# Kernel tuning notes

Hardware: AMD Instinct MI355X
Metric: run time of the kernel (lower is better)

The kernel has to match this reference:

```python
import jax, jax.numpy as jnp
import numpy as np

N = 16384
D = 512
NNZ = 163840
NUM_ITERS = 10


def setup_inputs() -> dict:
    key = jax.random.key(0)
    k1, k2, k3, k4 = jax.random.split(key, 4)
    x = jax.random.normal(k1, (N, D), dtype=jnp.float32)
    edge_val = jax.random.uniform(k2, (NNZ,), dtype=jnp.float32)
    edge_row = jnp.sort(jax.random.randint(k3, (NNZ,), 0, N, dtype=jnp.int32))
    edge_col = jax.random.randint(k4, (NNZ,), 0, N, dtype=jnp.int32)
    alpha = jnp.zeros((1,), dtype=jnp.float32)
    beta = jnp.zeros((1,), dtype=jnp.float32)
    sigma = jnp.ones((1,), dtype=jnp.float32)
    return {"x": x, "alpha": alpha, "beta": beta, "sigma": sigma,
            "edge_val": edge_val, "edge_row": edge_row, "edge_col": edge_col,
            "num_iters": NUM_ITERS}


def reference(x, alpha, beta, sigma, edge_val, edge_row, edge_col, num_iters):
    n = x.shape[0]
    # tf.nn.l2_normalize(x, axis=1)
    xn = x * jax.lax.rsqrt(jnp.maximum(jnp.sum(x * x, axis=1, keepdims=True), 1e-12))
    # cosine similarity only at sparse support positions; diagonal zeroed
    sim_e = jnp.sum(xn[edge_row] * xn[edge_col], axis=-1)          # [nnz]
    sim_e = jnp.where(edge_row == edge_col, 0.0, sim_e)
    s = jnp.exp(sigma[0])
    sigma_sq = 2.0 * s * s
    sim_e = jnp.exp(sim_e / (2.0 * sigma_sq))
    # support = sparse support elementwise * similarity
    sup = edge_val * sim_e                                          # [nnz]
    # row-sum of sparse support
    normalize = jax.ops.segment_sum(sup, edge_row, num_segments=n)  # [N]
    a = jnp.exp(alpha[0])
    b = jnp.exp(beta[0])
    denom = b + normalize[:, None] * a + a                          # [N,1] -> broadcast over D

    def step(out, _):
        # sparse matmul: (support @ out)
        Ax = jax.ops.segment_sum(sup[:, None] * out[edge_col], edge_row, num_segments=n)
        out = (x * b + (Ax + out) * a) / denom
        return out, None

    out, _ = jax.lax.scan(step, x, None, length=num_iters)
    return out
```

## Files before the change

kernel.cpp:

```cpp
#include <hip/hip_runtime.h>
#include <hip/hip_fp16.h>

#define DIM 512
#define N_ITERS 10

typedef float floatx2 __attribute__((ext_vector_type(2)));
typedef float fx4 __attribute__((ext_vector_type(4)));
typedef unsigned int ux4 __attribute__((ext_vector_type(4)));

__device__ __forceinline__ unsigned int pack2h(float lo, float hi) {
    __half2 h = __float22half2_rn(make_float2(lo, hi));
    return *reinterpret_cast<unsigned int*>(&h);
}
__device__ __forceinline__ float2 unpack2h(unsigned int u) {
    return __half22float2(*reinterpret_cast<__half2*>(&u));
}
__device__ __forceinline__ unsigned int pack4f8(float f0, float f1, float f2, float f3) {
    int v = 0;
    v = __builtin_amdgcn_cvt_pk_fp8_f32(f0, f1, v, false);
    v = __builtin_amdgcn_cvt_pk_fp8_f32(f2, f3, v, true);
    return (unsigned int)v;
}

__global__ void __launch_bounds__(256)
prep_kernel(const float* __restrict__ x,
            const float* __restrict__ alpha,
            const float* __restrict__ beta,
            const float* __restrict__ sigma,
            const int* __restrict__ erow, int nnz,
            float* __restrict__ consts,
            int* __restrict__ rstart,
            unsigned int* __restrict__ xc8,
            unsigned short* __restrict__ xbh, int n) {
    int tid = blockIdx.x * blockDim.x + threadIdx.x;
    float b = expf(beta[0]);
    if (tid == 0) {
        float a = expf(alpha[0]);
        float s = expf(sigma[0]);
        consts[0] = a;
        consts[1] = b;
        consts[2] = 1.0f / (4.0f * s * s);
    }
    if (tid <= n) {
        int lo = 0, hi = nnz;
        while (lo < hi) {
            int mid = (lo + hi) >> 1;
            if (erow[mid] < tid) lo = mid + 1; else hi = mid;
        }
        rstart[tid] = lo;
    }
    int wid = tid >> 6;
    int lane = tid & 63;
    if (wid >= n) return;
    const size_t base = (size_t)wid * DIM + lane * 8;
    const fx4* p = (const fx4*)(x + base);
    fx4 u = p[0];
    fx4 v = p[1];
    float s = u.x*u.x + u.y*u.y + u.z*u.z + u.w*u.w
            + v.x*v.x + v.y*v.y + v.z*v.z + v.w*v.w;
    ux4 hb;
    hb.x = pack2h(u.x * b, u.y * b); hb.y = pack2h(u.z * b, u.w * b);
    hb.z = pack2h(v.x * b, v.y * b); hb.w = pack2h(v.z * b, v.w * b);
    *(ux4*)(xbh + base) = hb;
    #pragma unroll
    for (int m = 32; m >= 1; m >>= 1) s += __shfl_xor(s, m, 64);
    float inr = rsqrtf(fmaxf(s, 1e-12f));
    ux4 q;
    q.x = pack4f8(u.x * inr, u.y * inr, u.z * inr, u.w * inr);
    q.y = pack4f8(v.x * inr, v.y * inr, v.z * inr, v.w * inr);
    q.z = pack4f8(u.x, u.y, u.z, u.w);
    q.w = pack4f8(v.x, v.y, v.z, v.w);
    *(ux4*)(xc8 + ((size_t)wid * 256 + lane * 4)) = q;
}

__device__ __forceinline__ float dot8f8(const float* A, unsigned int lo, unsigned int hi) {
    floatx2 p0 = __builtin_amdgcn_cvt_pk_f32_fp8((int)lo, false);
    floatx2 p1 = __builtin_amdgcn_cvt_pk_f32_fp8((int)lo, true);
    floatx2 p2 = __builtin_amdgcn_cvt_pk_f32_fp8((int)hi, false);
    floatx2 p3 = __builtin_amdgcn_cvt_pk_f32_fp8((int)hi, true);
    return A[0]*p0.x + A[1]*p0.y + A[2]*p1.x + A[3]*p1.y
         + A[4]*p2.x + A[5]*p2.y + A[6]*p3.x + A[7]*p3.y;
}

#define ACCP(lo, hi, w2)                                                          \
    do {                                                                          \
        acc0 += (w2) * __builtin_amdgcn_cvt_pk_f32_fp8((int)(lo), false);         \
        acc1 += (w2) * __builtin_amdgcn_cvt_pk_f32_fp8((int)(lo), true);          \
        acc2 += (w2) * __builtin_amdgcn_cvt_pk_f32_fp8((int)(hi), false);         \
        acc3 += (w2) * __builtin_amdgcn_cvt_pk_f32_fp8((int)(hi), true);          \
    } while (0)

__global__ void __launch_bounds__(256)
fused1_kernel(const unsigned int* __restrict__ xc8,
              const float* __restrict__ x,
              const float* __restrict__ eval_,
              const int* __restrict__ ecol,
              const int* __restrict__ rstart,
              const float* __restrict__ consts,
              float* __restrict__ sup, float* __restrict__ inv_denom,
              unsigned short* __restrict__ next16,
              unsigned int* __restrict__ next8, int n) {
    int row = (blockIdx.x * blockDim.x + threadIdx.x) >> 6;
    int lane = threadIdx.x & 63;
    if (row >= n) return;
    const size_t base = (size_t)row * DIM + lane * 8;
    ux4 hr = *(const ux4*)(xc8 + (size_t)row * 256 + lane * 4);
    const fx4* px = (const fx4*)(x + base);
    fx4 u = px[0];
    fx4 v = px[1];
    float A[8];
    {
        floatx2 p0 = __builtin_amdgcn_cvt_pk_f32_fp8((int)hr.x, false);
        floatx2 p1 = __builtin_amdgcn_cvt_pk_f32_fp8((int)hr.x, true);
        floatx2 p2 = __builtin_amdgcn_cvt_pk_f32_fp8((int)hr.y, false);
        floatx2 p3 = __builtin_amdgcn_cvt_pk_f32_fp8((int)hr.y, true);
        A[0]=p0.x; A[1]=p0.y; A[2]=p1.x; A[3]=p1.y;
        A[4]=p2.x; A[5]=p2.y; A[6]=p3.x; A[7]=p3.y;
    }
    float a = consts[0], b = consts[1], c2 = consts[2];
    int rs = rstart[row], re = rstart[row + 1];
    float norm_acc = 0.0f;
    floatx2 acc0 = {0.f, 0.f}, acc1 = {0.f, 0.f}, acc2 = {0.f, 0.f}, acc3 = {0.f, 0.f};
    int e = rs;
    for (; e + 3 < re; e += 4) {
        int c[4]; float ev[4]; ux4 h[4]; float s[4];
        #pragma unroll
        for (int j = 0; j < 4; ++j) { c[j] = ecol[e + j]; ev[j] = eval_[e + j]; }
        #pragma unroll
        for (int j = 0; j < 4; ++j)
            h[j] = *(const ux4*)(xc8 + (size_t)c[j] * 256 + lane * 4);
        #pragma unroll
        for (int j = 0; j < 4; ++j) s[j] = dot8f8(A, h[j].x, h[j].y);
        #pragma unroll
        for (int m = 32; m >= 1; m >>= 1) {
            #pragma unroll
            for (int j = 0; j < 4; ++j) s[j] += __shfl_xor(s[j], m, 64);
        }
        #pragma unroll
        for (int j = 0; j < 4; ++j) {
            float sim = (row == c[j]) ? 0.0f : s[j];
            float sp = ev[j] * expf(sim * c2);
            norm_acc += sp;
            if (lane == 0) sup[e + j] = sp;
            floatx2 w2 = {sp, sp};
            ACCP(h[j].z, h[j].w, w2);
        }
    }
    for (; e < re; ++e) {
        int c0 = ecol[e];
        float ev0 = eval_[e];
        ux4 h0 = *(const ux4*)(xc8 + (size_t)c0 * 256 + lane * 4);
        float s0 = dot8f8(A, h0.x, h0.y);
        #pragma unroll
        for (int m = 32; m >= 1; m >>= 1) s0 += __shfl_xor(s0, m, 64);
        float sim0 = (row == c0) ? 0.0f : s0;
        float sp0 = ev0 * expf(sim0 * c2);
        norm_acc += sp0;
        if (lane == 0) sup[e] = sp0;
        floatx2 w2 = {sp0, sp0};
        ACCP(h0.z, h0.w, w2);
    }
    float inv_d = 1.0f / (b + norm_acc * a + a);
    if (lane == 0) inv_denom[row] = inv_d;
    float r0 = (u.x * b + (acc0.x + u.x) * a) * inv_d;
    float r1 = (u.y * b + (acc0.y + u.y) * a) * inv_d;
    float r2 = (u.z * b + (acc1.x + u.z) * a) * inv_d;
    float r3 = (u.w * b + (acc1.y + u.w) * a) * inv_d;
    float r4 = (v.x * b + (acc2.x + v.x) * a) * inv_d;
    float r5 = (v.y * b + (acc2.y + v.y) * a) * inv_d;
    float r6 = (v.z * b + (acc3.x + v.z) * a) * inv_d;
    float r7 = (v.w * b + (acc3.y + v.w) * a) * inv_d;
    ux4 ho;
    ho.x = pack2h(r0, r1); ho.y = pack2h(r2, r3);
    ho.z = pack2h(r4, r5); ho.w = pack2h(r6, r7);
    *(ux4*)(next16 + base) = ho;
    uint2 q;
    q.x = pack4f8(r0, r1, r2, r3);
    q.y = pack4f8(r4, r5, r6, r7);
    *(uint2*)(next8 + (size_t)row * (DIM / 4) + lane * 2) = q;
}

__global__ void __launch_bounds__(256)
iter_kernel(const unsigned short* __restrict__ prev16,
            const unsigned int* __restrict__ prev8,
            unsigned short* __restrict__ next16,
            unsigned int* __restrict__ next8,
            float* __restrict__ out_f32, int last,
            const float* __restrict__ consts, const float* __restrict__ inv_denom,
            const float* __restrict__ sup, const int* __restrict__ ecol,
            const int* __restrict__ rstart,
            const unsigned short* __restrict__ xbh, int n) {
    int row = (blockIdx.x * blockDim.x + threadIdx.x) >> 6;
    int lane = threadIdx.x & 63;
    if (row >= n) return;
    const size_t loff16 = lane * 8;
    const size_t base16 = (size_t)row * DIM + loff16;
    const size_t loff8 = lane * 2;
    ux4 hs = *(const ux4*)(prev16 + base16);
    ux4 hx = *(const ux4*)(xbh + base16);
    float a = consts[0];
    float inv_d = inv_denom[row];
    int rs = rstart[row], re = rstart[row + 1];
    floatx2 acc0 = {0.f, 0.f}, acc1 = {0.f, 0.f}, acc2 = {0.f, 0.f}, acc3 = {0.f, 0.f};
    int e = rs;
    for (; e + 7 < re; e += 8) {
        int c[8]; float w[8]; uint2 h[8];
        #pragma unroll
        for (int j = 0; j < 8; ++j) { c[j] = ecol[e + j]; w[j] = sup[e + j]; }
        #pragma unroll
        for (int j = 0; j < 8; ++j)
            h[j] = *(const uint2*)(prev8 + (size_t)c[j] * (DIM / 4) + loff8);
        #pragma unroll
        for (int j = 0; j < 8; ++j) {
            floatx2 w2 = {w[j], w[j]};
            ACCP(h[j].x, h[j].y, w2);
        }
    }
    for (; e + 1 < re; e += 2) {
        int c0 = ecol[e], c1 = ecol[e + 1];
        float w0 = sup[e], w1 = sup[e + 1];
        uint2 h0 = *(const uint2*)(prev8 + (size_t)c0 * (DIM / 4) + loff8);
        uint2 h1 = *(const uint2*)(prev8 + (size_t)c1 * (DIM / 4) + loff8);
        floatx2 w20 = {w0, w0}; ACCP(h0.x, h0.y, w20);
        floatx2 w21 = {w1, w1}; ACCP(h1.x, h1.y, w21);
    }
    if (e < re) {
        float w = sup[e];
        int c = ecol[e];
        uint2 h = *(const uint2*)(prev8 + (size_t)c * (DIM / 4) + loff8);
        floatx2 w2 = {w, w}; ACCP(h.x, h.y, w2);
    }
    float2 s0 = unpack2h(hs.x), s1 = unpack2h(hs.y);
    float2 s2 = unpack2h(hs.z), s3 = unpack2h(hs.w);
    float2 x0 = unpack2h(hx.x), x1 = unpack2h(hx.y);
    float2 x2 = unpack2h(hx.z), x3 = unpack2h(hx.w);
    float r0 = (x0.x + (acc0.x + s0.x) * a) * inv_d;
    float r1 = (x0.y + (acc0.y + s0.y) * a) * inv_d;
    float r2 = (x1.x + (acc1.x + s1.x) * a) * inv_d;
    float r3 = (x1.y + (acc1.y + s1.y) * a) * inv_d;
    float r4 = (x2.x + (acc2.x + s2.x) * a) * inv_d;
    float r5 = (x2.y + (acc2.y + s2.y) * a) * inv_d;
    float r6 = (x3.x + (acc3.x + s3.x) * a) * inv_d;
    float r7 = (x3.y + (acc3.y + s3.y) * a) * inv_d;
    if (last) {
        fx4* o = (fx4*)(out_f32 + base16);
        fx4 o0 = {r0, r1, r2, r3};
        fx4 o1 = {r4, r5, r6, r7};
        o[0] = o0;
        o[1] = o1;
    } else {
        ux4 ho;
        ho.x = pack2h(r0, r1); ho.y = pack2h(r2, r3);
        ho.z = pack2h(r4, r5); ho.w = pack2h(r6, r7);
        *(ux4*)(next16 + base16) = ho;
        uint2 q;
        q.x = pack4f8(r0, r1, r2, r3);
        q.y = pack4f8(r4, r5, r6, r7);
        *(uint2*)(next8 + (size_t)row * (DIM / 4) + loff8) = q;
    }
}

extern "C" void kernel_launch(void* const* d_in, const int* in_sizes, int n_in,
                              void* d_out, int out_size, void* d_ws, size_t ws_size,
                              hipStream_t stream) {
    const float* x     = (const float*)d_in[0];
    const float* alpha = (const float*)d_in[1];
    const float* beta  = (const float*)d_in[2];
    const float* sigma = (const float*)d_in[3];
    const float* eval_ = (const float*)d_in[4];
    const int* erow = (const int*)d_in[5];
    const int* ecol = (const int*)d_in[6];

    const int n   = in_sizes[0] / DIM;
    const int nnz = in_sizes[4];

    float* ws        = (float*)d_ws;
    float* consts    = ws;
    float* inv_denom = ws + 64;
    int*   rstart    = (int*)(inv_denom + n);
    float* sup       = (float*)(rstart + n + 64);
    unsigned short* xbh    = (unsigned short*)(sup + nnz);
    unsigned short* bufB16 = xbh + (size_t)n * DIM;
    unsigned int*   xc8    = (unsigned int*)(bufB16 + (size_t)n * DIM);
    unsigned int*   bufB8  = xc8 + (size_t)n * 256;
    unsigned int*   bufA8  = xc8;
    unsigned short* bufA16 = (unsigned short*)d_out;
    float* out_f32 = (float*)d_out;

    prep_kernel<<<(n * 64) / 256, 256, 0, stream>>>(x, alpha, beta, sigma,
                                                    erow, nnz, consts, rstart,
                                                    xc8, xbh, n);
    fused1_kernel<<<(n * 64) / 256, 256, 0, stream>>>(xc8, x, eval_, ecol, rstart,
                                                      consts, sup, inv_denom,
                                                      bufB16, bufB8, n);
    for (int k = 0; k < N_ITERS - 1; ++k) {
        const unsigned short* prev16 = (k & 1) ? bufA16 : bufB16;
        const unsigned int*   prev8  = (k & 1) ? bufA8  : bufB8;
        unsigned short* next16 = (k & 1) ? bufB16 : bufA16;
        unsigned int*   next8  = (k & 1) ? bufB8  : bufA8;
        int last = (k == N_ITERS - 2) ? 1 : 0;
        iter_kernel<<<(n * 64) / 256, 256, 0, stream>>>(prev16, prev8, next16, next8,
                                                        out_f32, last,
                                                        consts, inv_denom, sup, ecol,
                                                        rstart, xbh, n);
    }
}
```

Before: 332.3 us.

## Split feature columns across XCD halves so each L2 caches half the gather set

```diff
diff --git a/kernel.cpp b/kernel.cpp
--- a/kernel.cpp
+++ b/kernel.cpp
@@ -6,6 +6,7 @@
 
 typedef float floatx2 __attribute__((ext_vector_type(2)));
 typedef float fx4 __attribute__((ext_vector_type(4)));
+typedef unsigned int ux2 __attribute__((ext_vector_type(2)));
 typedef unsigned int ux4 __attribute__((ext_vector_type(4)));
 
 __device__ __forceinline__ unsigned int pack2h(float lo, float hi) {
@@ -88,6 +89,12 @@
         acc1 += (w2) * __builtin_amdgcn_cvt_pk_f32_fp8((int)(lo), true);          \
         acc2 += (w2) * __builtin_amdgcn_cvt_pk_f32_fp8((int)(hi), false);         \
         acc3 += (w2) * __builtin_amdgcn_cvt_pk_f32_fp8((int)(hi), true);          \
+    } while (0)
+
+#define ACCP4(u, w2)                                                              \
+    do {                                                                          \
+        acc0 += (w2) * __builtin_amdgcn_cvt_pk_f32_fp8((int)(u), false);          \
+        acc1 += (w2) * __builtin_amdgcn_cvt_pk_f32_fp8((int)(u), true);           \
     } while (0)
 
 __global__ void __launch_bounds__(256)
@@ -190,73 +197,64 @@
             const float* __restrict__ sup, const int* __restrict__ ecol,
             const int* __restrict__ rstart,
             const unsigned short* __restrict__ xbh, int n) {
-    int row = (blockIdx.x * blockDim.x + threadIdx.x) >> 6;
+    int bid = blockIdx.x;
+    int xcd = bid & 7;
+    int pass = xcd >> 2;
+    int sub = xcd & 3;
+    int row_block = (bid >> 3) * 4 + sub;
+    int row = row_block * 4 + (threadIdx.x >> 6);
     int lane = threadIdx.x & 63;
     if (row >= n) return;
-    const size_t loff16 = lane * 8;
-    const size_t base16 = (size_t)row * DIM + loff16;
-    const size_t loff8 = lane * 2;
-    ux4 hs = *(const ux4*)(prev16 + base16);
-    ux4 hx = *(const ux4*)(xbh + base16);
+    const size_t e16 = (size_t)row * DIM + pass * (DIM / 2) + lane * 4;
+    const size_t g8 = (size_t)pass * (DIM / 8) + lane;
+    ux2 hs = __builtin_nontemporal_load((const ux2*)(prev16 + e16));
+    ux2 hx = __builtin_nontemporal_load((const ux2*)(xbh + e16));
     float a = consts[0];
     float inv_d = inv_denom[row];
     int rs = rstart[row], re = rstart[row + 1];
-    floatx2 acc0 = {0.f, 0.f}, acc1 = {0.f, 0.f}, acc2 = {0.f, 0.f}, acc3 = {0.f, 0.f};
+    floatx2 acc0 = {0.f, 0.f}, acc1 = {0.f, 0.f};
     int e = rs;
     for (; e + 7 < re; e += 8) {
-        int c[8]; float w[8]; uint2 h[8];
+        int c[8]; float w[8]; unsigned int h[8];
         #pragma unroll
         for (int j = 0; j < 8; ++j) { c[j] = ecol[e + j]; w[j] = sup[e + j]; }
         #pragma unroll
         for (int j = 0; j < 8; ++j)
-            h[j] = *(const uint2*)(prev8 + (size_t)c[j] * (DIM / 4) + loff8);
+            h[j] = prev8[(size_t)c[j] * (DIM / 4) + g8];
         #pragma unroll
         for (int j = 0; j < 8; ++j) {
             floatx2 w2 = {w[j], w[j]};
-            ACCP(h[j].x, h[j].y, w2);
+            ACCP4(h[j], w2);
         }
     }
     for (; e + 1 < re; e += 2) {
         int c0 = ecol[e], c1 = ecol[e + 1];
         float w0 = sup[e], w1 = sup[e + 1];
-        uint2 h0 = *(const uint2*)(prev8 + (size_t)c0 * (DIM / 4) + loff8);
-        uint2 h1 = *(const uint2*)(prev8 + (size_t)c1 * (DIM / 4) + loff8);
-        floatx2 w20 = {w0, w0}; ACCP(h0.x, h0.y, w20);
-        floatx2 w21 = {w1, w1}; ACCP(h1.x, h1.y, w21);
+        unsigned int h0 = prev8[(size_t)c0 * (DIM / 4) + g8];
+        unsigned int h1 = prev8[(size_t)c1 * (DIM / 4) + g8];
+        floatx2 w20 = {w0, w0}; ACCP4(h0, w20);
+        floatx2 w21 = {w1, w1}; ACCP4(h1, w21);
     }
     if (e < re) {
         float w = sup[e];
         int c = ecol[e];
-        uint2 h = *(const uint2*)(prev8 + (size_t)c * (DIM / 4) + loff8);
-        floatx2 w2 = {w, w}; ACCP(h.x, h.y, w2);
+        unsigned int h = prev8[(size_t)c * (DIM / 4) + g8];
+        floatx2 w2 = {w, w}; ACCP4(h, w2);
     }
     float2 s0 = unpack2h(hs.x), s1 = unpack2h(hs.y);
-    float2 s2 = unpack2h(hs.z), s3 = unpack2h(hs.w);
     float2 x0 = unpack2h(hx.x), x1 = unpack2h(hx.y);
-    float2 x2 = unpack2h(hx.z), x3 = unpack2h(hx.w);
     float r0 = (x0.x + (acc0.x + s0.x) * a) * inv_d;
     float r1 = (x0.y + (acc0.y + s0.y) * a) * inv_d;
     float r2 = (x1.x + (acc1.x + s1.x) * a) * inv_d;
     float r3 = (x1.y + (acc1.y + s1.y) * a) * inv_d;
-    float r4 = (x2.x + (acc2.x + s2.x) * a) * inv_d;
-    float r5 = (x2.y + (acc2.y + s2.y) * a) * inv_d;
-    float r6 = (x3.x + (acc3.x + s3.x) * a) * inv_d;
-    float r7 = (x3.y + (acc3.y + s3.y) * a) * inv_d;
     if (last) {
-        fx4* o = (fx4*)(out_f32 + base16);
-        fx4 o0 = {r0, r1, r2, r3};
-        fx4 o1 = {r4, r5, r6, r7};
-        o[0] = o0;
-        o[1] = o1;
+        fx4 o = {r0, r1, r2, r3};
+        *(fx4*)(out_f32 + e16) = o;
     } else {
-        ux4 ho;
+        ux2 ho;
         ho.x = pack2h(r0, r1); ho.y = pack2h(r2, r3);
-        ho.z = pack2h(r4, r5); ho.w = pack2h(r6, r7);
-        *(ux4*)(next16 + base16) = ho;
-        uint2 q;
-        q.x = pack4f8(r0, r1, r2, r3);
-        q.y = pack4f8(r4, r5, r6, r7);
-        *(uint2*)(next8 + (size_t)row * (DIM / 4) + loff8) = q;
+        *(ux2*)(next16 + e16) = ho;
+        next8[(size_t)row * (DIM / 4) + g8] = pack4f8(r0, r1, r2, r3);
     }
 }
 
@@ -293,15 +291,16 @@
     fused1_kernel<<<(n * 64) / 256, 256, 0, stream>>>(xc8, x, eval_, ecol, rstart,
                                                       consts, sup, inv_denom,
                                                       bufB16, bufB8, n);
+    const int iter_blocks = 2 * (n / 4);
     for (int k = 0; k < N_ITERS - 1; ++k) {
         const unsigned short* prev16 = (k & 1) ? bufA16 : bufB16;
         const unsigned int*   prev8  = (k & 1) ? bufA8  : bufB8;
         unsigned short* next16 = (k & 1) ? bufB16 : bufA16;
         unsigned int*   next8  = (k & 1) ? bufB8  : bufA8;
         int last = (k == N_ITERS - 2) ? 1 : 0;
-        iter_kernel<<<(n * 64) / 256, 256, 0, stream>>>(prev16, prev8, next16, next8,
-                                                        out_f32, last,
-                                                        consts, inv_denom, sup, ecol,
-                                                        rstart, xbh, n);
-    }
-}
+        iter_kernel<<<iter_blocks, 256, 0, stream>>>(prev16, prev8, next16, next8,
+                                                     out_f32, last,
+                                                     consts, inv_denom, sup, ecol,
+                                                     rstart, xbh, n);
+    }
+}
```

Result: slower. 357.3 us (+7.5%).
